# Kernel tuning notes

Measured on AMD Instinct MI355X. Metric: run time of the kernel, lower is better.

## Reference

```python
import jax, jax.numpy as jnp
import numpy as np

LATENT = 2000
N_GROUPS = 10000  # loci_count // window_size
KERNEL = 20       # window_size * 2; per-group input length is 1 so out length == KERNEL
BATCH = 128
EPS = 1e-5
SLOPE = 0.1


def setup_inputs() -> dict:
    key = jax.random.key(0)
    k1, k2, k3, k4, k5 = jax.random.split(key, 5)
    return {
        "z": jax.random.normal(k1, (BATCH, LATENT), dtype=jnp.float32),
        "W_fc": jax.random.normal(k2, (N_GROUPS, LATENT), dtype=jnp.float32) * 0.02,
        "b_fc": jax.random.normal(k3, (N_GROUPS,), dtype=jnp.float32) * 0.02,
        "gamma": jnp.ones((N_GROUPS,), dtype=jnp.float32),
        "beta": jnp.zeros((N_GROUPS,), dtype=jnp.float32),
        "conv_w": jax.random.normal(k4, (N_GROUPS, KERNEL), dtype=jnp.float32) * 0.1,
        "conv_b": jax.random.normal(k5, (N_GROUPS,), dtype=jnp.float32) * 0.02,
    }


def reference(z, W_fc, b_fc, gamma, beta, conv_w, conv_b):
    # Linear: (B, L) @ (L, G) -> (B, G)
    h = jnp.einsum("bl,gl->bg", z, W_fc) + b_fc
    # BatchNorm1d (training mode: biased batch statistics, eps=1e-5)
    mean = jnp.mean(h, axis=0)
    var = jnp.mean(jnp.square(h - mean), axis=0)
    h = (h - mean) * jax.lax.rsqrt(var + EPS) * gamma + beta
    h = jnp.where(h >= 0, h, SLOPE * h)  # LeakyReLU(0.1)
    # Grouped ConvTranspose1d with per-group input length 1 degenerates to
    # an outer product per channel: y[b,g,k] = h[b,g]*w[g,k] + b[g]
    y = h[:, :, None] * conv_w[None, :, :] + conv_b[None, :, None]  # (B, G, K)
    y = jnp.where(y >= 0, y, SLOPE * y)  # LeakyReLU(0.1)
    out = jax.nn.sigmoid(y.reshape(z.shape[0], N_GROUPS * KERNEL))
    return out
```

## Files before the change

### kernel.cpp

```cpp
#include <hip/hip_runtime.h>
#include <hip/hip_bf16.h>
#include <stdint.h>

#define BATCH 128
#define LAT   2000
#define NG    10000
#define KW    20
#define OUTW  (NG * KW)
#define EPSV  1e-5f

#define GT    64
#define BK    64
#define KSPL  4

#define EG        16
#define HR_STRIDE 132

typedef __bf16 bf16x8 __attribute__((ext_vector_type(8)));
typedef float  f32x4  __attribute__((ext_vector_type(4)));

__device__ __forceinline__ ushort f2bf(float f) {
  uint32_t u = __builtin_bit_cast(uint32_t, f);
  u = (u + 0x7FFFu + ((u >> 16) & 1u)) >> 16;
  return (ushort)u;
}

__device__ __forceinline__ int4 pack8(const float* p) {
  float4 f0 = *(const float4*)p;
  float4 f1 = *(const float4*)(p + 4);
  int4 v;
  v.x = (int)((uint32_t)f2bf(f0.x) | ((uint32_t)f2bf(f0.y) << 16));
  v.y = (int)((uint32_t)f2bf(f0.z) | ((uint32_t)f2bf(f0.w) << 16));
  v.z = (int)((uint32_t)f2bf(f1.x) | ((uint32_t)f2bf(f1.y) << 16));
  v.w = (int)((uint32_t)f2bf(f1.z) | ((uint32_t)f2bf(f1.w) << 16));
  return v;
}

__global__ __launch_bounds__(256, 4) void gemm_splitk_kernel(
    const float* __restrict__ zp, const float* __restrict__ wp,
    float* __restrict__ hp) {
  const int tid = threadIdx.x;
  const int g0  = blockIdx.x * GT;
  const int s   = blockIdx.y;
  const int kbase = s * 512;
  const int klen  = (s < 3) ? 512 : (LAT - 3 * 512);

  __shared__ ushort As[GT * BK];
  __shared__ ushort Bs[BATCH * BK];

  const int lane = tid & 63;
  const int w    = tid >> 6;
  const int wm   = w & 1;
  const int wn   = w >> 1;
  const int q    = lane >> 4;
  const int cl   = lane & 15;

  f32x4 acc[2][4];
  const f32x4 vzero = {0.f, 0.f, 0.f, 0.f};
#pragma unroll
  for (int i = 0; i < 2; ++i)
#pragma unroll
    for (int j = 0; j < 4; ++j) acc[i][j] = vzero;

  for (int it = 0; it < 8; ++it) {
    const int k0 = it * BK;
    __syncthreads();

#pragma unroll
    for (int i = 0; i < 2; ++i) {
      int c = i * 256 + tid;
      int r = c >> 3, sc = c & 7;
      int lk = k0 + sc * 8;
      int g  = g0 + r;
      int4 v = make_int4(0, 0, 0, 0);
      if (lk < klen && g < NG)
        v = pack8(wp + (size_t)g * LAT + kbase + lk);
      *(int4*)&As[r * BK + ((sc ^ (r & 7)) << 3)] = v;
    }
#pragma unroll
    for (int i = 0; i < 4; ++i) {
      int c = i * 256 + tid;
      int r = c >> 3, sc = c & 7;
      int lk = k0 + sc * 8;
      int4 v = make_int4(0, 0, 0, 0);
      if (lk < klen)
        v = pack8(zp + (size_t)r * LAT + kbase + lk);
      *(int4*)&Bs[r * BK + ((sc ^ (r & 7)) << 3)] = v;
    }
    __syncthreads();

#pragma unroll
    for (int kk = 0; kk < 2; ++kk) {
      int sc = kk * 4 + q;
      bf16x8 af[2], bfr[4];
#pragma unroll
      for (int mt = 0; mt < 2; ++mt) {
        int ra = wm * 32 + mt * 16 + cl;
        af[mt] = *(const bf16x8*)&As[ra * BK + ((sc ^ (ra & 7)) << 3)];
      }
#pragma unroll
      for (int nt = 0; nt < 4; ++nt) {
        int rb = wn * 64 + nt * 16 + cl;
        bfr[nt] = *(const bf16x8*)&Bs[rb * BK + ((sc ^ (rb & 7)) << 3)];
      }
#pragma unroll
      for (int mt = 0; mt < 2; ++mt)
#pragma unroll
        for (int nt = 0; nt < 4; ++nt)
          acc[mt][nt] = __builtin_amdgcn_mfma_f32_16x16x32_bf16(
              af[mt], bfr[nt], acc[mt][nt], 0, 0, 0);
    }
  }

  float* base = hp + (size_t)s * NG * BATCH;
#pragma unroll
  for (int mt = 0; mt < 2; ++mt) {
#pragma unroll
    for (int r = 0; r < 4; ++r) {
      int g = g0 + wm * 32 + mt * 16 + q * 4 + r;
      if (g < NG) {
#pragma unroll
        for (int nt = 0; nt < 4; ++nt) {
          int b = wn * 64 + nt * 16 + cl;
          base[(size_t)g * BATCH + b] = acc[mt][nt][r];
        }
      }
    }
  }
}

__global__ __launch_bounds__(256, 4) void bn_expand_kernel(
    const float* __restrict__ hp, const float* __restrict__ gammap,
    const float* __restrict__ betap, const float* __restrict__ convwp,
    const float* __restrict__ convbp, float* __restrict__ out) {
  const int tid = threadIdx.x;
  const int g0  = blockIdx.x * EG;

  __shared__ float  h_raw[EG * HR_STRIDE];
  __shared__ float4 cw_s[EG * 5];
  __shared__ float  cb_s[EG];
  __shared__ float  scale_s[EG];
  __shared__ float  shift_s[EG];

  if (tid < EG * 5)
    cw_s[tid] = *(const float4*)(convwp + (size_t)g0 * KW + tid * 4);
  if (tid < EG) cb_s[tid] = convbp[g0 + tid];

  float sm[2], sq[2];
#pragma unroll
  for (int half = 0; half < 2; ++half) {
    const int idx = tid + half * 256;
    const int gl  = idx >> 5;
    const int bb  = (idx & 31) * 4;
    float4 a = make_float4(0.f, 0.f, 0.f, 0.f);
#pragma unroll
    for (int s = 0; s < KSPL; ++s) {
      const float4 v =
          *(const float4*)(hp + ((size_t)s * NG + g0 + gl) * BATCH + bb);
      a.x += v.x; a.y += v.y; a.z += v.z; a.w += v.w;
    }
    *(float4*)&h_raw[gl * HR_STRIDE + bb] = a;
    sm[half] = a.x + a.y + a.z + a.w;
    sq[half] = a.x * a.x + a.y * a.y + a.z * a.z + a.w * a.w;
  }
#pragma unroll
  for (int m = 1; m < 32; m <<= 1) {
    sm[0] += __shfl_xor(sm[0], m); sq[0] += __shfl_xor(sq[0], m);
    sm[1] += __shfl_xor(sm[1], m); sq[1] += __shfl_xor(sq[1], m);
  }
  if ((tid & 31) == 0) {
#pragma unroll
    for (int half = 0; half < 2; ++half) {
      const int gl = (tid >> 5) + half * 8;
      float mean = sm[half] * (1.f / 128.f);
      float var  = sq[half] * (1.f / 128.f) - mean * mean;
      var = (var < 0.f) ? 0.f : var;
      float inv   = __builtin_amdgcn_rsqf(var + EPSV);
      float scale = inv * gammap[g0 + gl];
      scale_s[gl] = scale;
      shift_s[gl] = betap[g0 + gl] - mean * scale;
    }
  }
  __syncthreads();

  if (tid < 240) {
    const int col4 = tid % 80;
    const int r0   = tid / 80;
    const int gl   = col4 / 5;
    const float4 w4  = cw_s[col4];
    const float  cb  = cb_s[gl];
    const float  scl = scale_s[gl];
    const float  sft = shift_s[gl];
    const float* hsrc = &h_raw[gl * HR_STRIDE];
    float* obase = out + (size_t)g0 * KW + (size_t)col4 * 4;
    for (int j = 0; j < 43; ++j) {
      const int row = j * 3 + r0;
      if (row < BATCH) {
        float h = hsrc[row];
        h = fmaf(h, scl, sft);
        h = fmaxf(h, h * 0.1f);
        float y0 = fmaf(h, w4.x, cb);
        float y1 = fmaf(h, w4.y, cb);
        float y2 = fmaf(h, w4.z, cb);
        float y3 = fmaf(h, w4.w, cb);
        y0 = fmaxf(y0, y0 * 0.1f);
        y1 = fmaxf(y1, y1 * 0.1f);
        y2 = fmaxf(y2, y2 * 0.1f);
        y3 = fmaxf(y3, y3 * 0.1f);
        float4 ov;
        ov.x = __builtin_amdgcn_rcpf(1.f + exp2f(y0 * -1.44269504f));
        ov.y = __builtin_amdgcn_rcpf(1.f + exp2f(y1 * -1.44269504f));
        ov.z = __builtin_amdgcn_rcpf(1.f + exp2f(y2 * -1.44269504f));
        ov.w = __builtin_amdgcn_rcpf(1.f + exp2f(y3 * -1.44269504f));
        *(float4*)(obase + (size_t)row * OUTW) = ov;
      }
    }
  }
}

__global__ __launch_bounds__(256, 2) void fused_decoder_kernel(
    const float* __restrict__ zp, const float* __restrict__ wp,
    const float* __restrict__ gammap, const float* __restrict__ betap,
    const float* __restrict__ convwp, const float* __restrict__ convbp,
    float* __restrict__ out) {
  const int tid = threadIdx.x;
  const int g0  = blockIdx.x * 32;

  __shared__ ushort As[BATCH * BK];
  __shared__ ushort Bs[32 * BK];
  __shared__ float statS[2][2][16];
  __shared__ float statQ[2][2][16];

  const int lane = tid & 63;
  const int w    = tid >> 6;
  const int wm   = w & 1;
  const int wn   = w >> 1;
  const int q    = lane >> 4;
  const int cl   = lane & 15;

  f32x4 acc[4];
  const f32x4 vzero = {0.f, 0.f, 0.f, 0.f};
#pragma unroll
  for (int i = 0; i < 4; ++i) acc[i] = vzero;

  for (int it = 0; it < 32; ++it) {
    const int k0 = it * BK;
    __syncthreads();
#pragma unroll
    for (int i = 0; i < 4; ++i) {
      int c = i * 256 + tid;
      int r = c >> 3, sc = c & 7;
      int gk = k0 + sc * 8;
      int4 v = make_int4(0, 0, 0, 0);
      if (gk < LAT) v = pack8(zp + (size_t)r * LAT + gk);
      *(int4*)&As[r * BK + ((sc ^ (r & 7)) << 3)] = v;
    }
    {
      int r = tid >> 3, sc = tid & 7;
      int g  = g0 + r;
      int gk = k0 + sc * 8;
      int4 v = make_int4(0, 0, 0, 0);
      if (gk < LAT && g < NG) v = pack8(wp + (size_t)g * LAT + gk);
      *(int4*)&Bs[r * BK + ((sc ^ (r & 7)) << 3)] = v;
    }
    __syncthreads();
#pragma unroll
    for (int kk = 0; kk < 2; ++kk) {
      int sc = kk * 4 + q;
      bf16x8 af[4], bfr;
#pragma unroll
      for (int mt = 0; mt < 4; ++mt) {
        int ra = wm * 64 + mt * 16 + cl;
        af[mt] = *(const bf16x8*)&As[ra * BK + ((sc ^ (ra & 7)) << 3)];
      }
      {
        int rb = wn * 16 + cl;
        bfr = *(const bf16x8*)&Bs[rb * BK + ((sc ^ (rb & 7)) << 3)];
      }
#pragma unroll
      for (int mt = 0; mt < 4; ++mt)
        acc[mt] = __builtin_amdgcn_mfma_f32_16x16x32_bf16(af[mt], bfr,
                                                          acc[mt], 0, 0, 0);
    }
  }

  float s = 0.f, ss = 0.f;
#pragma unroll
  for (int mt = 0; mt < 4; ++mt)
#pragma unroll
    for (int r = 0; r < 4; ++r) {
      float v = acc[mt][r];
      s += v; ss += v * v;
    }
  s += __shfl_xor(s, 16); ss += __shfl_xor(ss, 16);
  s += __shfl_xor(s, 32); ss += __shfl_xor(ss, 32);
  if (q == 0) { statS[wm][wn][cl] = s; statQ[wm][wn][cl] = ss; }
  __syncthreads();

  const int gcol = g0 + wn * 16 + cl;
  const int gc   = (gcol < NG) ? gcol : (NG - 1);
  float S = statS[0][wn][cl] + statS[1][wn][cl];
  float Q = statQ[0][wn][cl] + statQ[1][wn][cl];
  float mean = S * (1.f / 128.f);
  float var  = Q * (1.f / 128.f) - mean * mean;
  var = (var < 0.f) ? 0.f : var;
  float inv = __builtin_amdgcn_rsqf(var + EPSV);
  float ga = gammap[gc], be = betap[gc], cb = convbp[gc];
  float wv[KW];
  {
    const float4* pw = (const float4*)(convwp + (size_t)gc * KW);
#pragma unroll
    for (int j = 0; j < 5; ++j) {
      float4 f = pw[j];
      wv[4 * j] = f.x; wv[4 * j + 1] = f.y;
      wv[4 * j + 2] = f.z; wv[4 * j + 3] = f.w;
    }
  }
  float scale = inv * ga;
  float shift = be - mean * scale;
  const bool ok = (gcol < NG);
#pragma unroll
  for (int mt = 0; mt < 4; ++mt) {
#pragma unroll
    for (int r = 0; r < 4; ++r) {
      float h = acc[mt][r] * scale + shift;
      h = fmaxf(h, h * 0.1f);
      int b = wm * 64 + mt * 16 + q * 4 + r;
      float4 ov[5];
#pragma unroll
      for (int j = 0; j < 5; ++j) {
        float y0 = h * wv[4 * j]     + cb;
        float y1 = h * wv[4 * j + 1] + cb;
        float y2 = h * wv[4 * j + 2] + cb;
        float y3 = h * wv[4 * j + 3] + cb;
        y0 = fmaxf(y0, y0 * 0.1f);
        y1 = fmaxf(y1, y1 * 0.1f);
        y2 = fmaxf(y2, y2 * 0.1f);
        y3 = fmaxf(y3, y3 * 0.1f);
        ov[j].x = __builtin_amdgcn_rcpf(1.f + exp2f(y0 * -1.44269504f));
        ov[j].y = __builtin_amdgcn_rcpf(1.f + exp2f(y1 * -1.44269504f));
        ov[j].z = __builtin_amdgcn_rcpf(1.f + exp2f(y2 * -1.44269504f));
        ov[j].w = __builtin_amdgcn_rcpf(1.f + exp2f(y3 * -1.44269504f));
      }
      if (ok) {
        float4* po = (float4*)(out + (size_t)b * OUTW + (size_t)gcol * KW);
#pragma unroll
        for (int j = 0; j < 5; ++j) po[j] = ov[j];
      }
    }
  }
}

extern "C" void kernel_launch(void* const* d_in, const int* in_sizes, int n_in,
                              void* d_out, int out_size, void* d_ws, size_t ws_size,
                              hipStream_t stream) {
  const float* z     = (const float*)d_in[0];
  const float* W     = (const float*)d_in[1];
  const float* gamma = (const float*)d_in[3];
  const float* beta  = (const float*)d_in[4];
  const float* convw = (const float*)d_in[5];
  const float* convb = (const float*)d_in[6];
  float* out = (float*)d_out;

  const size_t hp_elems = (size_t)KSPL * NG * BATCH;
  const size_t need = hp_elems * sizeof(float);

  if (ws_size >= need) {
    float* hp = (float*)d_ws;
    dim3 g1((NG + GT - 1) / GT, KSPL);
    gemm_splitk_kernel<<<g1, 256, 0, stream>>>(z, W, hp);
    bn_expand_kernel<<<NG / EG, 256, 0, stream>>>(hp, gamma, beta, convw,
                                                  convb, out);
  } else {
    fused_decoder_kernel<<<(NG + 31) / 32, 256, 0, stream>>>(
        z, W, gamma, beta, convw, convb, out);
  }
}
```

Measured before the change: 206.2 us.

## Pre-swizzle z to bf16 and stream it into LDS via global_load_lds

A small prep kernel now converts z to bf16 once per call and stores it in the swizzled tile layout the GEMM expects. The GEMM then copies each z tile straight from global memory into LDS with global_load_lds, so every block no longer repeats the fp32-to-bf16 packing of the batch operand. The split-K factor also doubles from 4 to 8 with 256-wide segments, giving more blocks for parallelism. The cost is an extra kernel launch, extra workspace, and twice as many partial sums for the BN stage to write and read.

After: 214.9 us. +4.2%, slower.

```diff
diff --git a/kernel.cpp b/kernel.cpp
--- a/kernel.cpp
+++ b/kernel.cpp
@@ -11,7 +11,9 @@
 
 #define GT    64
 #define BK    64
-#define KSPL  4
+#define KSPL  8
+#define KSEG  256
+#define NKT   32
 
 #define EG        16
 #define HR_STRIDE 132
@@ -36,17 +38,39 @@
   return v;
 }
 
+__device__ __forceinline__ void gload_lds16(const void* g, void* l) {
+  __builtin_amdgcn_global_load_lds(
+      (const __attribute__((address_space(1))) unsigned int*)g,
+      (__attribute__((address_space(3))) unsigned int*)l, 16, 0, 0);
+}
+
+__global__ __launch_bounds__(256) void zprep_kernel(
+    const float* __restrict__ zp, int4* __restrict__ zswz) {
+  const int kt  = blockIdx.x;
+  const int tid = threadIdx.x;
+#pragma unroll
+  for (int i = 0; i < 4; ++i) {
+    int c = i * 256 + tid;
+    int r = c >> 3, j = c & 7;
+    int sc = j ^ (r & 7);
+    int k0 = kt * 64 + sc * 8;
+    int4 v = make_int4(0, 0, 0, 0);
+    if (k0 < LAT) v = pack8(zp + (size_t)r * LAT + k0);
+    zswz[(size_t)kt * 1024 + c] = v;
+  }
+}
+
 __global__ __launch_bounds__(256, 4) void gemm_splitk_kernel(
-    const float* __restrict__ zp, const float* __restrict__ wp,
+    const int4* __restrict__ zswz, const float* __restrict__ wp,
     float* __restrict__ hp) {
   const int tid = threadIdx.x;
   const int g0  = blockIdx.x * GT;
   const int s   = blockIdx.y;
-  const int kbase = s * 512;
-  const int klen  = (s < 3) ? 512 : (LAT - 3 * 512);
-
-  __shared__ ushort As[GT * BK];
-  __shared__ ushort Bs[BATCH * BK];
+  const int kbase = s * KSEG;
+  const int klen  = (s < KSPL - 1) ? KSEG : (LAT - (KSPL - 1) * KSEG);
+
+  __shared__ __attribute__((aligned(16))) ushort As[GT * BK];
+  __shared__ __attribute__((aligned(16))) ushort Bs[BATCH * BK];
 
   const int lane = tid & 63;
   const int w    = tid >> 6;
@@ -62,9 +86,16 @@
 #pragma unroll
     for (int j = 0; j < 4; ++j) acc[i][j] = vzero;
 
-  for (int it = 0; it < 8; ++it) {
+  for (int it = 0; it < KSEG / BK; ++it) {
     const int k0 = it * BK;
     __syncthreads();
+
+    const int4* zt = zswz + (size_t)(s * (KSEG / BK) + it) * 1024;
+#pragma unroll
+    for (int i = 0; i < 4; ++i) {
+      int c = i * 256 + tid;
+      gload_lds16(zt + c, &Bs[c * 8]);
+    }
 
 #pragma unroll
     for (int i = 0; i < 2; ++i) {
@@ -76,16 +107,6 @@
       if (lk < klen && g < NG)
         v = pack8(wp + (size_t)g * LAT + kbase + lk);
       *(int4*)&As[r * BK + ((sc ^ (r & 7)) << 3)] = v;
-    }
-#pragma unroll
-    for (int i = 0; i < 4; ++i) {
-      int c = i * 256 + tid;
-      int r = c >> 3, sc = c & 7;
-      int lk = k0 + sc * 8;
-      int4 v = make_int4(0, 0, 0, 0);
-      if (lk < klen)
-        v = pack8(zp + (size_t)r * LAT + kbase + lk);
-      *(int4*)&Bs[r * BK + ((sc ^ (r & 7)) << 3)] = v;
     }
     __syncthreads();
 
@@ -362,13 +383,18 @@
   const float* convb = (const float*)d_in[6];
   float* out = (float*)d_out;
 
-  const size_t hp_elems = (size_t)KSPL * NG * BATCH;
-  const size_t need = hp_elems * sizeof(float);
+  const size_t hp_elems   = (size_t)KSPL * NG * BATCH;
+  const size_t hp_bytes   = hp_elems * sizeof(float);
+  const size_t zswz_bytes = (size_t)NKT * 1024 * 16;
+  const size_t need = hp_bytes + zswz_bytes;
 
   if (ws_size >= need) {
-    float* hp = (float*)d_ws;
+    float* hp   = (float*)d_ws;
+    int4* zswz  = (int4*)((char*)d_ws + hp_bytes);
+
+    zprep_kernel<<<NKT, 256, 0, stream>>>(z, zswz);
     dim3 g1((NG + GT - 1) / GT, KSPL);
-    gemm_splitk_kernel<<<g1, 256, 0, stream>>>(z, W, hp);
+    gemm_splitk_kernel<<<g1, 256, 0, stream>>>(zswz, W, hp);
     bn_expand_kernel<<<NG / EG, 256, 0, stream>>>(hp, gamma, beta, convw,
                                                   convb, out);
   } else {
```

## Fuse GEMM with batchnorm expand using pre-swizzled bf16 z and direct LDS loads

Applied to the files above, without the earlier changes.

Removes the split-K GEMM kernel and its 4x partial-sum workspace round trip. A small prep kernel converts z to bf16 once, in the swizzled tile layout. The fused kernel then computes each 16-group block's full-K product, streaming z tiles into LDS with global_load_lds, and runs the batchnorm/expand epilogue directly from LDS. The trade-off is that every block re-reads the whole bf16 z (about 0.5 MB) from L2. It also has only 16 groups per block with small MFMA work per sync, which may leave the loop latency-bound.

Result: faster. 196.1 us (-4.9%).

```diff
diff --git a/kernel.cpp b/kernel.cpp
--- a/kernel.cpp
+++ b/kernel.cpp
@@ -9,9 +9,8 @@
 #define OUTW  (NG * KW)
 #define EPSV  1e-5f
 
-#define GT    64
 #define BK    64
-#define KSPL  4
+#define NKT   32
 
 #define EG        16
 #define HR_STRIDE 132
@@ -36,106 +35,35 @@
   return v;
 }
 
-__global__ __launch_bounds__(256, 4) void gemm_splitk_kernel(
-    const float* __restrict__ zp, const float* __restrict__ wp,
-    float* __restrict__ hp) {
-  const int tid = threadIdx.x;
-  const int g0  = blockIdx.x * GT;
-  const int s   = blockIdx.y;
-  const int kbase = s * 512;
-  const int klen  = (s < 3) ? 512 : (LAT - 3 * 512);
-
-  __shared__ ushort As[GT * BK];
-  __shared__ ushort Bs[BATCH * BK];
-
-  const int lane = tid & 63;
-  const int w    = tid >> 6;
-  const int wm   = w & 1;
-  const int wn   = w >> 1;
-  const int q    = lane >> 4;
-  const int cl   = lane & 15;
-
-  f32x4 acc[2][4];
-  const f32x4 vzero = {0.f, 0.f, 0.f, 0.f};
-#pragma unroll
-  for (int i = 0; i < 2; ++i)
-#pragma unroll
-    for (int j = 0; j < 4; ++j) acc[i][j] = vzero;
-
-  for (int it = 0; it < 8; ++it) {
-    const int k0 = it * BK;
-    __syncthreads();
-
-#pragma unroll
-    for (int i = 0; i < 2; ++i) {
-      int c = i * 256 + tid;
-      int r = c >> 3, sc = c & 7;
-      int lk = k0 + sc * 8;
-      int g  = g0 + r;
-      int4 v = make_int4(0, 0, 0, 0);
-      if (lk < klen && g < NG)
-        v = pack8(wp + (size_t)g * LAT + kbase + lk);
-      *(int4*)&As[r * BK + ((sc ^ (r & 7)) << 3)] = v;
-    }
-#pragma unroll
-    for (int i = 0; i < 4; ++i) {
-      int c = i * 256 + tid;
-      int r = c >> 3, sc = c & 7;
-      int lk = k0 + sc * 8;
-      int4 v = make_int4(0, 0, 0, 0);
-      if (lk < klen)
-        v = pack8(zp + (size_t)r * LAT + kbase + lk);
-      *(int4*)&Bs[r * BK + ((sc ^ (r & 7)) << 3)] = v;
-    }
-    __syncthreads();
-
-#pragma unroll
-    for (int kk = 0; kk < 2; ++kk) {
-      int sc = kk * 4 + q;
-      bf16x8 af[2], bfr[4];
-#pragma unroll
-      for (int mt = 0; mt < 2; ++mt) {
-        int ra = wm * 32 + mt * 16 + cl;
-        af[mt] = *(const bf16x8*)&As[ra * BK + ((sc ^ (ra & 7)) << 3)];
-      }
-#pragma unroll
-      for (int nt = 0; nt < 4; ++nt) {
-        int rb = wn * 64 + nt * 16 + cl;
-        bfr[nt] = *(const bf16x8*)&Bs[rb * BK + ((sc ^ (rb & 7)) << 3)];
-      }
-#pragma unroll
-      for (int mt = 0; mt < 2; ++mt)
-#pragma unroll
-        for (int nt = 0; nt < 4; ++nt)
-          acc[mt][nt] = __builtin_amdgcn_mfma_f32_16x16x32_bf16(
-              af[mt], bfr[nt], acc[mt][nt], 0, 0, 0);
-    }
-  }
-
-  float* base = hp + (size_t)s * NG * BATCH;
-#pragma unroll
-  for (int mt = 0; mt < 2; ++mt) {
-#pragma unroll
-    for (int r = 0; r < 4; ++r) {
-      int g = g0 + wm * 32 + mt * 16 + q * 4 + r;
-      if (g < NG) {
-#pragma unroll
-        for (int nt = 0; nt < 4; ++nt) {
-          int b = wn * 64 + nt * 16 + cl;
-          base[(size_t)g * BATCH + b] = acc[mt][nt][r];
-        }
-      }
-    }
-  }
-}
-
-__global__ __launch_bounds__(256, 4) void bn_expand_kernel(
-    const float* __restrict__ hp, const float* __restrict__ gammap,
-    const float* __restrict__ betap, const float* __restrict__ convwp,
-    const float* __restrict__ convbp, float* __restrict__ out) {
+__device__ __forceinline__ void gload_lds16(const void* g, void* l) {
+  __builtin_amdgcn_global_load_lds(
+      (const __attribute__((address_space(1))) unsigned int*)g,
+      (__attribute__((address_space(3))) unsigned int*)l, 16, 0, 0);
+}
+
+__global__ __launch_bounds__(256) void zprep_kernel(
+    const float* __restrict__ zp, int4* __restrict__ zswz) {
+  const int cg = blockIdx.x * 256 + threadIdx.x;
+  const int kt = cg >> 10;
+  const int c  = cg & 1023;
+  const int r  = c >> 3, j = c & 7;
+  const int sc = j ^ (r & 7);
+  const int k0 = kt * 64 + sc * 8;
+  int4 v = make_int4(0, 0, 0, 0);
+  if (k0 < LAT) v = pack8(zp + (size_t)r * LAT + k0);
+  zswz[cg] = v;
+}
+
+__global__ __launch_bounds__(256, 4) void fused16_kernel(
+    const int4* __restrict__ zswz, const float* __restrict__ wp,
+    const float* __restrict__ gammap, const float* __restrict__ betap,
+    const float* __restrict__ convwp, const float* __restrict__ convbp,
+    float* __restrict__ out) {
   const int tid = threadIdx.x;
   const int g0  = blockIdx.x * EG;
 
+  __shared__ __attribute__((aligned(16))) ushort Zs[BATCH * BK];
+  __shared__ __attribute__((aligned(16))) ushort Ws[EG * BK];
   __shared__ float  h_raw[EG * HR_STRIDE];
   __shared__ float4 cw_s[EG * 5];
   __shared__ float  cb_s[EG];
@@ -146,20 +74,61 @@
     cw_s[tid] = *(const float4*)(convwp + (size_t)g0 * KW + tid * 4);
   if (tid < EG) cb_s[tid] = convbp[g0 + tid];
 
+  const int lane = tid & 63;
+  const int w    = tid >> 6;
+  const int q    = lane >> 4;
+  const int cl   = lane & 15;
+
+  f32x4 acc[2];
+  const f32x4 vzero = {0.f, 0.f, 0.f, 0.f};
+  acc[0] = vzero; acc[1] = vzero;
+
+  for (int it = 0; it < NKT; ++it) {
+    __syncthreads();
+
+    const int4* zt = zswz + (size_t)it * 1024;
+#pragma unroll
+    for (int i = 0; i < 4; ++i) {
+      int c = i * 256 + tid;
+      gload_lds16(zt + c, &Zs[c * 8]);
+    }
+    if (tid < 128) {
+      int r = tid >> 3, j = tid & 7;
+      int gk = it * BK + j * 8;
+      int4 v = make_int4(0, 0, 0, 0);
+      if (gk < LAT) v = pack8(wp + (size_t)(g0 + r) * LAT + gk);
+      *(int4*)&Ws[r * BK + ((j ^ (r & 7)) << 3)] = v;
+    }
+    __syncthreads();
+
+#pragma unroll
+    for (int kk = 0; kk < 2; ++kk) {
+      int sc = kk * 4 + q;
+      bf16x8 af = *(const bf16x8*)&Ws[cl * BK + ((sc ^ (cl & 7)) << 3)];
+#pragma unroll
+      for (int nt = 0; nt < 2; ++nt) {
+        int rb = w * 32 + nt * 16 + cl;
+        bf16x8 bfr = *(const bf16x8*)&Zs[rb * BK + ((sc ^ (rb & 7)) << 3)];
+        acc[nt] = __builtin_amdgcn_mfma_f32_16x16x32_bf16(af, bfr, acc[nt],
+                                                          0, 0, 0);
+      }
+    }
+  }
+
+#pragma unroll
+  for (int nt = 0; nt < 2; ++nt)
+#pragma unroll
+    for (int r = 0; r < 4; ++r)
+      h_raw[(q * 4 + r) * HR_STRIDE + w * 32 + nt * 16 + cl] = acc[nt][r];
+  __syncthreads();
+
   float sm[2], sq[2];
 #pragma unroll
   for (int half = 0; half < 2; ++half) {
     const int idx = tid + half * 256;
     const int gl  = idx >> 5;
     const int bb  = (idx & 31) * 4;
-    float4 a = make_float4(0.f, 0.f, 0.f, 0.f);
-#pragma unroll
-    for (int s = 0; s < KSPL; ++s) {
-      const float4 v =
-          *(const float4*)(hp + ((size_t)s * NG + g0 + gl) * BATCH + bb);
-      a.x += v.x; a.y += v.y; a.z += v.z; a.w += v.w;
-    }
-    *(float4*)&h_raw[gl * HR_STRIDE + bb] = a;
+    const float4 a = *(const float4*)&h_raw[gl * HR_STRIDE + bb];
     sm[half] = a.x + a.y + a.z + a.w;
     sq[half] = a.x * a.x + a.y * a.y + a.z * a.z + a.w * a.w;
   }
@@ -362,15 +331,13 @@
   const float* convb = (const float*)d_in[6];
   float* out = (float*)d_out;
 
-  const size_t hp_elems = (size_t)KSPL * NG * BATCH;
-  const size_t need = hp_elems * sizeof(float);
-
-  if (ws_size >= need) {
-    float* hp = (float*)d_ws;
-    dim3 g1((NG + GT - 1) / GT, KSPL);
-    gemm_splitk_kernel<<<g1, 256, 0, stream>>>(z, W, hp);
-    bn_expand_kernel<<<NG / EG, 256, 0, stream>>>(hp, gamma, beta, convw,
-                                                  convb, out);
+  const size_t zswz_bytes = (size_t)NKT * 1024 * 16;
+
+  if (ws_size >= zswz_bytes) {
+    int4* zswz = (int4*)d_ws;
+    zprep_kernel<<<128, 256, 0, stream>>>(z, zswz);
+    fused16_kernel<<<NG / EG, 256, 0, stream>>>(zswz, W, gamma, beta,
+                                                convw, convb, out);
   } else {
     fused_decoder_kernel<<<(NG + 31) / 32, 256, 0, stream>>>(
         z, W, gamma, beta, convw, convb, out);
```
